# Performance work log

Hardware: AMD Instinct MI355X
Metric: run time of the kernel (lower is better)

## Reference

```python
import jax, jax.numpy as jnp
import numpy as np
import math

N_QUBITS = 10
N_LAYERS = 2
HIDDEN = 768
VOCAB = 30522
DIM = 2 ** N_QUBITS


def _cnot_perm(c, t, n):
    # PennyLane convention: wire 0 is the most significant bit of the basis index.
    idx = np.arange(2 ** n)
    ctrl_bit = (idx >> (n - 1 - c)) & 1
    return jnp.asarray(idx ^ (ctrl_bit << (n - 1 - t)))

# BasicEntanglerLayers uses a CNOT ring: (0,1),(1,2),...,(n-1,0)
CNOT_PERMS = [_cnot_perm(q, (q + 1) % N_QUBITS, N_QUBITS) for q in range(N_QUBITS)]


def _apply_rx(state, theta, q):
    # state: (N, 2^n) complex, theta: (N,) per-sample RX angle on wire q.
    c = jnp.cos(theta * 0.5)[:, None, None]
    s = jnp.sin(theta * 0.5)[:, None, None]
    st = state.reshape(-1, 2 ** q, 2, DIM // (2 ** (q + 1)))
    a0, a1 = st[:, :, 0, :], st[:, :, 1, :]
    b0 = c * a0 - 1j * s * a1
    b1 = c * a1 - 1j * s * a0
    return jnp.stack([b0, b1], axis=2).reshape(state.shape)


def _quantum_probs(angles):
    # angles: (N, L, n). BasicEntanglerLayers = per-layer RX rotations + CNOT ring,
    # followed by qml.probs over all wires -> (N, 2^n).
    N = angles.shape[0]
    state = jnp.zeros((N, DIM), jnp.complex64).at[:, 0].set(1.0)
    for l in range(N_LAYERS):
        for q in range(N_QUBITS):
            state = _apply_rx(state, angles[:, l, q], q)
        for q in range(N_QUBITS):
            state = state[:, CNOT_PERMS[q]]
    return state.real ** 2 + state.imag ** 2


def _gelu(x):
    return x * 0.5 * (1.0 + jax.scipy.special.erf(x / math.sqrt(2.0)))


def setup_inputs() -> dict:
    key = jax.random.key(0)
    ks = jax.random.split(key, 4)
    B, S = 8, 512
    return {
        "hidden_states": jax.random.normal(ks[0], (B, S, HIDDEN), jnp.float32),
        "dense_w": jax.random.normal(ks[1], (HIDDEN, HIDDEN), jnp.float32) * 0.02,
        "dense_b": jnp.zeros((HIDDEN,), jnp.float32),
        "ln_w": jnp.ones((HIDDEN,), jnp.float32),
        "ln_b": jnp.zeros((HIDDEN,), jnp.float32),
        "ent_w": jax.random.normal(ks[2], (HIDDEN, N_LAYERS * N_QUBITS), jnp.float32) * 0.02,
        "ent_b": jnp.zeros((N_LAYERS * N_QUBITS,), jnp.float32),
        "proj_w": jax.random.normal(ks[3], (DIM, VOCAB), jnp.float32) * 0.02,
        "proj_b": jnp.zeros((VOCAB,), jnp.float32),
    }


def reference(hidden_states, dense_w, dense_b, ln_w, ln_b, ent_w, ent_b, proj_w, proj_b):
    # BertPredictionHeadTransform: dense -> gelu -> LayerNorm (eps inside sqrt)
    h = _gelu(hidden_states @ dense_w + dense_b)
    u = h.mean(-1, keepdims=True)
    v = ((h - u) ** 2).mean(-1, keepdims=True)
    h = ln_w * ((h - u) / jnp.sqrt(v + 1e-12)) + ln_b
    # entangle params -> sigmoid * 2pi, flatten batch to (N, L, n)
    ang = jax.nn.sigmoid(h @ ent_w + ent_b).reshape(-1, N_LAYERS, N_QUBITS) * (2.0 * math.pi)
    probs = _quantum_probs(ang)  # (B*S, 2^n)
    return probs @ proj_w + proj_b  # (B*S, vocab)
```

## Files before the change

### kernel.cpp

```cpp
#include <hip/hip_runtime.h>
#include <hip/hip_bf16.h>
#include <math.h>

#define HIDDEN 768
#define NROWS 4096
#define QDIM 1024
#define VOCAB 30522
#define NPAD 30592
#define NBX 239
#define NBY 32
#define NWG (NBX * NBY)
#define NT (QDIM / 64)

typedef _Float16 half8 __attribute__((ext_vector_type(8)));
typedef float floatx4 __attribute__((ext_vector_type(4)));

__device__ __forceinline__ void gload16(const _Float16* g, _Float16* l) {
  __builtin_amdgcn_global_load_lds(
      (const __attribute__((address_space(1))) void*)g,
      (__attribute__((address_space(3))) void*)l, 16, 0, 0);
}

__global__ __launch_bounds__(1024) void convert_transpose(
    const float* __restrict__ B, _Float16* __restrict__ BT) {
  __shared__ _Float16 tile[32][33];
  int n0 = blockIdx.x * 32;
  int k0 = blockIdx.y * 32;
  int tx = threadIdx.x, ty = threadIdx.y;
  int n = n0 + tx, k = k0 + ty;
  float v = (n < VOCAB) ? B[k * VOCAB + n] : 0.0f;
  tile[ty][tx] = (_Float16)v;
  __syncthreads();
  BT[(n0 + ty) * QDIM + (k0 + tx)] = tile[tx][ty];
}

__global__ __launch_bounds__(256) void gemm1_gelu(
    const float* __restrict__ A, const float* __restrict__ W,
    const float* __restrict__ bias, float* __restrict__ H) {
  __shared__ float As[64][17];
  __shared__ float Bs[16][68];
  int t = threadIdx.x;
  int bm = blockIdx.y * 64, bn = blockIdx.x * 64;
  int tx = t & 15, ty = t >> 4;
  float acc[4][4] = {};
  for (int k0 = 0; k0 < HIDDEN; k0 += 16) {
    {
      int r = t >> 2, c = (t & 3) * 4;
      float4 v = *(const float4*)&A[(bm + r) * HIDDEN + k0 + c];
      As[r][c] = v.x; As[r][c + 1] = v.y; As[r][c + 2] = v.z; As[r][c + 3] = v.w;
    }
    {
      int kr = t >> 4, c = (t & 15) * 4;
      float4 v = *(const float4*)&W[(k0 + kr) * HIDDEN + bn + c];
      Bs[kr][c] = v.x; Bs[kr][c + 1] = v.y; Bs[kr][c + 2] = v.z; Bs[kr][c + 3] = v.w;
    }
    __syncthreads();
#pragma unroll
    for (int k = 0; k < 16; k++) {
      float a[4], b[4];
#pragma unroll
      for (int i = 0; i < 4; i++) a[i] = As[ty * 4 + i][k];
#pragma unroll
      for (int j = 0; j < 4; j++) b[j] = Bs[k][tx * 4 + j];
#pragma unroll
      for (int i = 0; i < 4; i++)
#pragma unroll
        for (int j = 0; j < 4; j++) acc[i][j] += a[i] * b[j];
    }
    __syncthreads();
  }
#pragma unroll
  for (int i = 0; i < 4; i++) {
    int m = bm + ty * 4 + i;
#pragma unroll
    for (int j = 0; j < 4; j++) {
      int n = bn + tx * 4 + j;
      float x = acc[i][j] + bias[n];
      float g = x * 0.5f * (1.0f + erff(x * 0.70710678118654752f));
      H[m * HIDDEN + n] = g;
    }
  }
}

__device__ inline float block_sum256(float v, float* red) {
  int t = threadIdx.x;
#pragma unroll
  for (int o = 32; o > 0; o >>= 1) v += __shfl_down(v, o);
  __syncthreads();
  if ((t & 63) == 0) red[t >> 6] = v;
  __syncthreads();
  return red[0] + red[1] + red[2] + red[3];
}

__global__ __launch_bounds__(256) void row_quantum(
    const float* __restrict__ H, const float* __restrict__ ln_w,
    const float* __restrict__ ln_b, const float* __restrict__ ent_w,
    const float* __restrict__ ent_b, _Float16* __restrict__ probsA) {
  __shared__ float hn[HIDDEN];
  __shared__ float red[4];
  __shared__ float sr[QDIM];
  __shared__ float si[QDIM];
  __shared__ float ang[20];
  int t = threadIdx.x;
  int row = blockIdx.x;
  const float* hr = H + row * HIDDEN;

  float sum = 0.f;
  for (int i = t; i < HIDDEN; i += 256) {
    float v = hr[i];
    hn[i] = v;
    sum += v;
  }
  float u = block_sum256(sum, red) * (1.0f / HIDDEN);
  float vs = 0.f;
  for (int i = t; i < HIDDEN; i += 256) {
    float d = hn[i] - u;
    vs += d * d;
  }
  float var = block_sum256(vs, red) * (1.0f / HIDDEN);
  float inv = rsqrtf(var + 1e-12f);
  for (int i = t; i < HIDDEN; i += 256)
    hn[i] = ln_w[i] * ((hn[i] - u) * inv) + ln_b[i];
  __syncthreads();

  if (t < 20) {
    float acc = ent_b[t];
#pragma unroll 4
    for (int i = 0; i < HIDDEN; i++) acc += hn[i] * ent_w[i * 20 + t];
    float s = 1.0f / (1.0f + expf(-acc));
    ang[t] = 6.283185307179586f * s;
  }
  __syncthreads();

  for (int i = t; i < QDIM; i += 256) {
    sr[i] = (i == 0) ? 1.0f : 0.0f;
    si[i] = 0.0f;
  }
  __syncthreads();

  for (int l = 0; l < 2; l++) {
    for (int q = 0; q < 10; q++) {
      float th = ang[l * 10 + q] * 0.5f;
      float c = cosf(th), s = sinf(th);
      int bp = 9 - q;
      int mask = 1 << bp;
#pragma unroll
      for (int p = 0; p < 2; p++) {
        int pi = t + p * 256;
        int i0 = ((pi >> bp) << (bp + 1)) | (pi & (mask - 1));
        int i1 = i0 | mask;
        float a0r = sr[i0], a0i = si[i0], a1r = sr[i1], a1i = si[i1];
        sr[i0] = c * a0r + s * a1i;
        si[i0] = c * a0i - s * a1r;
        sr[i1] = c * a1r + s * a0i;
        si[i1] = c * a1i - s * a0r;
      }
      __syncthreads();
    }
    float tr[4], ti[4];
#pragma unroll
    for (int p = 0; p < 4; p++) {
      int i = t + p * 256;
      int j = i;
#pragma unroll
      for (int q = 9; q >= 0; q--) {
        int cb = 9 - q;
        int tb = 9 - ((q + 1) % 10);
        j ^= ((j >> cb) & 1) << tb;
      }
      tr[p] = sr[j];
      ti[p] = si[j];
    }
    __syncthreads();
#pragma unroll
    for (int p = 0; p < 4; p++) {
      int i = t + p * 256;
      sr[i] = tr[p];
      si[i] = ti[p];
    }
    __syncthreads();
  }

  for (int i = t; i < QDIM; i += 256) {
    float pv = sr[i] * sr[i] + si[i] * si[i];
    probsA[row * QDIM + i] = (_Float16)pv;
  }
}

__global__ __launch_bounds__(256) void gemm2_mfma(
    const _Float16* __restrict__ A,
    const _Float16* __restrict__ BT,
    const float* __restrict__ bias,
    float* __restrict__ C) {
  __shared__ _Float16 As[2][128][64];
  __shared__ _Float16 Bs[2][128][64];

  int t = threadIdx.x;
  int lane = t & 63, wave = t >> 6;
  int quad = lane >> 4, ln = lane & 15;
  int wm = (wave >> 1) * 64, wn = (wave & 1) * 64;

  int wg = blockIdx.x;
  int swz = (wg & 7) * (NWG / 8) + (wg >> 3);
  int bn = (swz >> 5) * 128;
  int bm = (swz & 31) * 128;

  int srow = t >> 3;
  int ps = t & 7;
  int lslot = ps ^ (srow & 7);
  const _Float16* gA = A  + (size_t)(bm + srow) * QDIM + lslot * 8;
  const _Float16* gB = BT + (size_t)(bn + srow) * QDIM + lslot * 8;

  int r7 = ln & 7;
  int off0 = ((0 * 4 + quad) ^ r7) * 8;
  int off1 = ((1 * 4 + quad) ^ r7) * 8;

  floatx4 acc[4][4];
#pragma unroll
  for (int i = 0; i < 4; i++)
#pragma unroll
    for (int j = 0; j < 4; j++) acc[i][j] = (floatx4){0.f, 0.f, 0.f, 0.f};

  auto STAGE = [&](int kt, int b) {
#pragma unroll
    for (int i = 0; i < 4; i++) {
      gload16(gA + (size_t)i * 32 * QDIM + kt * 64, &As[b][srow + i * 32][ps * 8]);
      gload16(gB + (size_t)i * 32 * QDIM + kt * 64, &Bs[b][srow + i * 32][ps * 8]);
    }
  };

  auto COMPUTE = [&](int b) {
    __builtin_amdgcn_s_setprio(1);
#pragma unroll
    for (int s = 0; s < 2; s++) {
      int off = s ? off1 : off0;
      half8 a[4], bb[4];
#pragma unroll
      for (int i = 0; i < 4; i++) a[i] = *(const half8*)&As[b][wm + i * 16 + ln][off];
#pragma unroll
      for (int j = 0; j < 4; j++) bb[j] = *(const half8*)&Bs[b][wn + j * 16 + ln][off];
#pragma unroll
      for (int i = 0; i < 4; i++)
#pragma unroll
        for (int j = 0; j < 4; j++)
          acc[i][j] = __builtin_amdgcn_mfma_f32_16x16x32_f16(a[i], bb[j], acc[i][j], 0, 0, 0);
    }
    __builtin_amdgcn_s_setprio(0);
  };

  STAGE(0, 0);
  int cur = 0;
  for (int kt = 0; kt < NT - 1; ++kt) {
    STAGE(kt + 1, cur ^ 1);
    asm volatile("s_waitcnt vmcnt(8)" ::: "memory");
    __builtin_amdgcn_s_barrier();
    COMPUTE(cur);
    __builtin_amdgcn_s_barrier();
    cur ^= 1;
  }
  asm volatile("s_waitcnt vmcnt(0)" ::: "memory");
  __builtin_amdgcn_s_barrier();
  COMPUTE(cur);

#pragma unroll
  for (int j = 0; j < 4; j++) {
    int n = bn + wn + j * 16 + ln;
    if (n >= VOCAB) continue;
    float bv = bias[n];
#pragma unroll
    for (int i = 0; i < 4; i++) {
#pragma unroll
      for (int r = 0; r < 4; r++) {
        int m = bm + wm + i * 16 + quad * 4 + r;
        C[(size_t)m * VOCAB + n] = acc[i][j][r] + bv;
      }
    }
  }
}

extern "C" void kernel_launch(void* const* d_in, const int* in_sizes, int n_in,
                              void* d_out, int out_size, void* d_ws, size_t ws_size,
                              hipStream_t stream) {
  const float* hs      = (const float*)d_in[0];
  const float* dense_w = (const float*)d_in[1];
  const float* dense_b = (const float*)d_in[2];
  const float* ln_w    = (const float*)d_in[3];
  const float* ln_b    = (const float*)d_in[4];
  const float* ent_w   = (const float*)d_in[5];
  const float* ent_b   = (const float*)d_in[6];
  const float* proj_w  = (const float*)d_in[7];
  const float* proj_b  = (const float*)d_in[8];
  float* out = (float*)d_out;

  char* ws = (char*)d_ws;
  float*     h      = (float*)ws;
  _Float16*  probsA = (_Float16*)(ws + 12582912);
  _Float16*  BT     = (_Float16*)(ws + 20971520);

  hipLaunchKernelGGL(convert_transpose, dim3(NPAD / 32, QDIM / 32), dim3(32, 32), 0, stream,
                     proj_w, BT);
  hipLaunchKernelGGL(gemm1_gelu, dim3(HIDDEN / 64, NROWS / 64), dim3(256), 0, stream,
                     hs, dense_w, dense_b, h);
  hipLaunchKernelGGL(row_quantum, dim3(NROWS), dim3(256), 0, stream,
                     h, ln_w, ln_b, ent_w, ent_b, probsA);
  hipLaunchKernelGGL(gemm2_mfma, dim3(NWG), dim3(256), 0, stream,
                     probsA, BT, proj_b, out);
}
```

Before: 1.281 ms.

## Stage GEMM output through LDS for coalesced nontemporal stores; parallelize entangle projection

The GEMM epilogue now writes the 128x128 accumulator tile into LDS (reusing the A/B staging buffer) and then stores it row-contiguously as float2 nontemporal writes with bias added, instead of scattered per-element stores. The goal is better coalescing of the large output write (4096x30522 floats). A slow path with per-element bounds checks handles the last column tile. Separately, the 20-output entangle projection is spread across all four waves with shuffle reductions instead of using 20 serial threads. The cost is two extra barriers and an LDS round trip in the epilogue.

```diff
diff --git a/kernel.cpp b/kernel.cpp
--- a/kernel.cpp
+++ b/kernel.cpp
@@ -14,6 +14,7 @@
 
 typedef _Float16 half8 __attribute__((ext_vector_type(8)));
 typedef float floatx4 __attribute__((ext_vector_type(4)));
+typedef float floatx2 __attribute__((ext_vector_type(2)));
 
 __device__ __forceinline__ void gload16(const _Float16* g, _Float16* l) {
   __builtin_amdgcn_global_load_lds(
@@ -123,12 +124,23 @@
     hn[i] = ln_w[i] * ((hn[i] - u) * inv) + ln_b[i];
   __syncthreads();
 
-  if (t < 20) {
-    float acc = ent_b[t];
-#pragma unroll 4
-    for (int i = 0; i < HIDDEN; i++) acc += hn[i] * ent_w[i * 20 + t];
-    float s = 1.0f / (1.0f + expf(-acc));
-    ang[t] = 6.283185307179586f * s;
+  {
+    int w = t >> 6, lane = t & 63;
+#pragma unroll
+    for (int kk = 0; kk < 5; kk++) {
+      int o = w * 5 + kk;
+      float p = 0.f;
+#pragma unroll
+      for (int i = 0; i < HIDDEN / 64; i++)
+        p += hn[lane + i * 64] * ent_w[(lane + i * 64) * 20 + o];
+#pragma unroll
+      for (int off = 32; off > 0; off >>= 1) p += __shfl_down(p, off);
+      if (lane == 0) {
+        float acc = p + ent_b[o];
+        float s = 1.0f / (1.0f + expf(-acc));
+        ang[o] = 6.283185307179586f * s;
+      }
+    }
   }
   __syncthreads();
 
@@ -192,8 +204,9 @@
     const _Float16* __restrict__ BT,
     const float* __restrict__ bias,
     float* __restrict__ C) {
-  __shared__ _Float16 As[2][128][64];
-  __shared__ _Float16 Bs[2][128][64];
+  __shared__ __align__(16) char smem_raw[65536];
+  auto As = (_Float16 (*)[128][64])(smem_raw);
+  auto Bs = (_Float16 (*)[128][64])(smem_raw + 32768);
 
   int t = threadIdx.x;
   int lane = t & 63, wave = t >> 6;
@@ -262,17 +275,37 @@
   __builtin_amdgcn_s_barrier();
   COMPUTE(cur);
 
-#pragma unroll
-  for (int j = 0; j < 4; j++) {
-    int n = bn + wn + j * 16 + ln;
-    if (n >= VOCAB) continue;
-    float bv = bias[n];
-#pragma unroll
-    for (int i = 0; i < 4; i++) {
-#pragma unroll
-      for (int r = 0; r < 4; r++) {
-        int m = bm + wm + i * 16 + quad * 4 + r;
-        C[(size_t)m * VOCAB + n] = acc[i][j][r] + bv;
+  __syncthreads();
+  float* ctile = (float*)smem_raw;
+#pragma unroll
+  for (int j = 0; j < 4; j++)
+#pragma unroll
+    for (int i = 0; i < 4; i++)
+#pragma unroll
+      for (int r = 0; r < 4; r++)
+        ctile[(wm + i * 16 + quad * 4 + r) * 128 + wn + j * 16 + ln] = acc[i][j][r];
+  __syncthreads();
+
+  if (bn + 128 <= VOCAB) {
+#pragma unroll 4
+    for (int idx = t; idx < 8192; idx += 256) {
+      int row = idx >> 6;
+      int c2 = (idx & 63) * 2;
+      floatx2 v = *(const floatx2*)&ctile[row * 128 + c2];
+      floatx2 bv = *(const floatx2*)&bias[bn + c2];
+      v[0] += bv[0]; v[1] += bv[1];
+      __builtin_nontemporal_store(
+          v, (floatx2*)&C[(size_t)(bm + row) * VOCAB + bn + c2]);
+    }
+  } else {
+    for (int idx = t; idx < 8192; idx += 256) {
+      int row = idx >> 6;
+      int c2 = (idx & 63) * 2;
+#pragma unroll
+      for (int e = 0; e < 2; e++) {
+        int n = bn + c2 + e;
+        if (n < VOCAB)
+          C[(size_t)(bm + row) * VOCAB + n] = ctile[row * 128 + c2 + e] + bias[n];
       }
     }
   }
```

Measured after the change: 1.143 ms. 10.8% less time.
